# Kernel tuning notes

Hardware: AMD Instinct MI355X
Metric: run time of the kernel (lower is better)

The kernel has to match this reference:

```python
import jax, jax.numpy as jnp
import numpy as np

B, L, D, H = 1, 2048, 1024, 16
d = D // H  # head dim = 64


def setup_inputs() -> dict:
    key = jax.random.key(0)
    ks = jax.random.split(key, 8)
    s = 1.0 / np.sqrt(D)
    return {
        "x": jax.random.normal(ks[0], (B, L, D), jnp.float32),
        "Wqkv_w": (jax.random.normal(ks[1], (D, 3 * D), jnp.float32) * s),
        "Wqkv_b": jnp.zeros((3 * D,), jnp.float32),
        "out_w": (jax.random.normal(ks[2], (D, D), jnp.float32) * s),
        "out_b": jnp.zeros((D,), jnp.float32),
        "W_static": jnp.zeros((H, d, d), jnp.float32),
        "Lambda_raw": jax.random.uniform(ks[3], (H, d, d), jnp.float32, -3.0, 3.0),
        "Gamma": jax.random.uniform(ks[4], (H, d, d), jnp.float32, -0.5 / np.sqrt(d), 0.5 / np.sqrt(d)),
        "gate_w1": (jax.random.normal(ks[5], (D, D // 2), jnp.float32) * s),
        "gate_b1": jnp.zeros((D // 2,), jnp.float32),
        "gate_w2": (jax.random.normal(ks[6], (D // 2, H), jnp.float32) * (1.0 / np.sqrt(D // 2))),
        "gate_b2": jnp.zeros((H,), jnp.float32),
    }


def _forward(x, Wqkv_w, Wqkv_b, out_w, out_b, W_static, Lambda_raw, Gamma,
             gate_w1, gate_b1, gate_w2, gate_b2):
    Bb, Ll, Dm = x.shape
    Hh = Gamma.shape[0]
    dd = Dm // Hh
    scale = 1.0 / np.sqrt(dd)

    # qkv projection: (B,L,3D) -> (3, B, H, L, d) layout
    qkv = (x @ Wqkv_w + Wqkv_b).reshape(Bb, Ll, 3, Hh, dd)
    q = jnp.transpose(qkv[:, :, 0], (0, 2, 1, 3))  # (B,H,L,d)
    k = jnp.transpose(qkv[:, :, 1], (0, 2, 1, 3))
    v = jnp.transpose(qkv[:, :, 2], (0, 2, 1, 3))

    # --- softmax branch (causal, additive -10000 mask like the original) ---
    scores = jnp.einsum('bhid,bhjd->bhij', q, k) * scale
    causal_mask = jnp.triu(jnp.full((Ll, Ll), -10000.0, dtype=scores.dtype), 1)
    attn = jax.nn.softmax(scores + causal_mask, axis=-1)
    y_softmax = jnp.einsum('bhij,bhjd->bhid', attn, v)

    # --- STP branch: linear recurrence over time via lax.scan ---
    retention = 1.0 - jax.nn.sigmoid(Lambda_raw)  # (H,d,d)
    k_stp = k * scale

    def step(state, inp):
        q_t, k_t, v_t = inp  # each (B,H,d)
        hebbian = v_t[..., :, None] * k_t[..., None, :]          # (B,H,d,d)
        state = retention * state + Gamma * hebbian              # (B,H,d,d)
        y_t = jnp.einsum('bhij,bhj->bhi', W_static + state, q_t)  # (B,H,d)
        return state, y_t

    state0 = jnp.zeros((Bb, Hh, dd, dd), x.dtype)
    qT = jnp.moveaxis(q, 2, 0)      # (L,B,H,d)
    kT = jnp.moveaxis(k_stp, 2, 0)
    vT = jnp.moveaxis(v, 2, 0)
    _, ys = jax.lax.scan(step, state0, (qT, kT, vT))
    y_stp = jnp.moveaxis(ys, 0, 2)  # (B,H,L,d)

    # --- learned gate: Linear -> GELU(exact) -> Linear -> sigmoid ---
    g = jax.nn.gelu(x @ gate_w1 + gate_b1, approximate=False)
    alpha = jax.nn.sigmoid(g @ gate_w2 + gate_b2)        # (B,L,H)
    alpha = jnp.transpose(alpha, (0, 2, 1))[..., None]   # (B,H,L,1)

    y = alpha * y_softmax + (1.0 - alpha) * y_stp        # (B,H,L,d)
    y = jnp.transpose(y, (0, 2, 1, 3)).reshape(Bb, Ll, Dm)
    return y @ out_w + out_b


def reference(x, Wqkv_w, Wqkv_b, out_w, out_b, W_static, Lambda_raw, Gamma,
              gate_w1, gate_b1, gate_w2, gate_b2):
    return _forward(x, Wqkv_w, Wqkv_b, out_w, out_b, W_static, Lambda_raw,
                    Gamma, gate_w1, gate_b1, gate_w2, gate_b2)
```

## Files before the change

### kernel.cpp

```cpp
#include <hip/hip_runtime.h>
#include <hip/hip_bf16.h>

#define L_SEQ 2048
#define DMODEL 1024
#define NHEAD 16
#define DHEAD 64
#define D3 3072

typedef __attribute__((ext_vector_type(8))) short s8v;
typedef __attribute__((ext_vector_type(4))) float f4v;
typedef unsigned int u32;
#define AS1 __attribute__((address_space(1)))
#define AS3 __attribute__((address_space(3)))

__device__ __forceinline__ short f2bf(float f) {
  __hip_bfloat16 h = __float2bfloat16(f);
  return *reinterpret_cast<short*>(&h);
}
__device__ __forceinline__ float bf2f(short s) {
  return __uint_as_float(((u32)(unsigned short)s) << 16);
}
__device__ __forceinline__ int pack2bf(float lo, float hi) {
  return (int)(((unsigned)(unsigned short)f2bf(hi) << 16) |
               (unsigned)(unsigned short)f2bf(lo));
}

__global__ __launch_bounds__(256) void conv_x(const float* __restrict__ x,
                                              short* __restrict__ xb)
{
  int i = (blockIdx.x * 256 + threadIdx.x) * 4;
  float4 v = *(const float4*)(x + i);
  short4 o;
  o.x = f2bf(v.x); o.y = f2bf(v.y); o.z = f2bf(v.z); o.w = f2bf(v.w);
  *(short4*)(xb + i) = o;
}

__global__ __launch_bounds__(256) void transpose_conv(const float* __restrict__ W,
    short* __restrict__ Wt, int K, int N)
{
  __shared__ float T[32][33];
  int bx = blockIdx.x, by = blockIdx.y;
  int col = threadIdx.x & 31, rb = threadIdx.x >> 5;
  #pragma unroll
  for (int it = 0; it < 4; ++it) {
    int r = it * 8 + rb;
    T[r][col] = W[(size_t)(by * 32 + r) * N + bx * 32 + col];
  }
  __syncthreads();
  #pragma unroll
  for (int it = 0; it < 4; ++it) {
    int r = it * 8 + rb;
    Wt[(size_t)(bx * 32 + r) * K + by * 32 + col] = f2bf(T[col][r]);
  }
}

__global__ __launch_bounds__(256) void conv_vt(const float* __restrict__ Vf,
                                               short* __restrict__ Vtb)
{
  int kb = blockIdx.x, h = blockIdx.y;
  int tid = threadIdx.x;
  __shared__ float Vs[64][65];
  for (int idx = tid; idx < 2048; idx += 256) {
    int key = idx >> 5, e2 = idx & 31;
    float2 vv = *(const float2*)(Vf + (size_t)(kb * 64 + key) * 1024 + h * 64 + e2 * 2);
    Vs[key][e2 * 2] = vv.x; Vs[key][e2 * 2 + 1] = vv.y;
  }
  __syncthreads();
  for (int idx = tid; idx < 2048; idx += 256) {
    int dim = idx >> 5, k2 = idx & 31;
    *(int*)&Vtb[((size_t)h * 64 + dim) * 2048 + kb * 64 + k2 * 2] =
        pack2bf(Vs[k2 * 2][dim], Vs[k2 * 2 + 1][dim]);
  }
}

template<int BM, int BN, int MODE>
__global__ __launch_bounds__(256, 6) void gemm_mfma(
    const short* __restrict__ A, const short* __restrict__ Bt,
    const float* __restrict__ bias, const float* __restrict__ bias2,
    float* __restrict__ C, short* __restrict__ C2,
    short* __restrict__ QbP, short* __restrict__ KbP,
    int M, int N, int K)
{
  constexpr int LA = BM / 64, LB = BN / 64;
  constexpr int WM = BM / 2, WN = BN / 2;
  constexpr int MT = WM / 16, NT = WN / 16;
  __shared__ __align__(16) short As[2][BM * 32];
  __shared__ __align__(16) short Bs[2][BN * 32];
  const int tid = threadIdx.x;
  const int w = tid >> 6, lane = tid & 63;
  const int quad = lane >> 4, c = lane & 15;
  const int m0 = blockIdx.y * BM, n0 = blockIdx.x * BN;
  const int wm = (w & 1) * WM, wn = (w >> 1) * WN;
  f4v acc[MT][NT] = {};

  auto stage = [&](int buf, int k0) {
    #pragma unroll
    for (int it = 0; it < LA; ++it) {
      int off = (it * 256 + tid) * 16;
      int row = off >> 6, colh = (off & 63) >> 1;
      __builtin_amdgcn_global_load_lds(
          (const AS1 u32*)(A + (size_t)(m0 + row) * K + k0 + colh),
          (AS3 u32*)(&As[buf][0] + (off >> 1)), 16, 0, 0);
    }
    #pragma unroll
    for (int it = 0; it < LB; ++it) {
      int off = (it * 256 + tid) * 16;
      int row = off >> 6, colh = (off & 63) >> 1;
      __builtin_amdgcn_global_load_lds(
          (const AS1 u32*)(Bt + (size_t)(n0 + row) * K + k0 + colh),
          (AS3 u32*)(&Bs[buf][0] + (off >> 1)), 16, 0, 0);
    }
  };
  stage(0, 0);
  int cur = 0;
  for (int k0 = 0; k0 < K; k0 += 32) {
    __syncthreads();
    if (k0 + 32 < K) stage(cur ^ 1, k0 + 32);
    s8v af[MT], bf[NT];
    #pragma unroll
    for (int mt = 0; mt < MT; ++mt)
      af[mt] = *(s8v*)&As[cur][(wm + mt * 16 + c) * 32 + quad * 8];
    #pragma unroll
    for (int nt = 0; nt < NT; ++nt)
      bf[nt] = *(s8v*)&Bs[cur][(wn + nt * 16 + c) * 32 + quad * 8];
    #pragma unroll
    for (int mt = 0; mt < MT; ++mt)
      #pragma unroll
      for (int nt = 0; nt < NT; ++nt)
        acc[mt][nt] = __builtin_amdgcn_mfma_f32_16x16x32_bf16(
            af[mt], bf[nt], acc[mt][nt], 0, 0, 0);
    cur ^= 1;
  }
  #pragma unroll
  for (int mt = 0; mt < MT; ++mt)
    #pragma unroll
    for (int r = 0; r < 4; ++r) {
      int m = m0 + wm + mt * 16 + quad * 4 + r;
      #pragma unroll
      for (int nt = 0; nt < NT; ++nt) {
        int n = n0 + wn + nt * 16 + c;
        float v = acc[mt][nt][r];
        if (MODE == 0) {
          C[(size_t)m * N + n] = v + bias[n];
        } else {
          if (n < 2048) {
            float v2 = v + bias[n];
            int hh = (n >> 6) & 15, ee = n & 63;
            short* dst = (n < 1024) ? QbP : KbP;
            dst[((size_t)hh * 2048 + m) * 64 + ee] = f2bf(v2);
          } else if (n < 3072) {
            C[(size_t)m * 1024 + (n - 2048)] = v + bias[n];
          } else {
            float t = v + bias2[n - 3072];
            t = 0.5f * t * (1.0f + erff(t * 0.70710678118654752f));
            C2[(size_t)m * 512 + (n - 3072)] = f2bf(t);
          }
        }
      }
    }
}

__global__ __launch_bounds__(256) void attn_mfma(
    const short* __restrict__ Qb, const short* __restrict__ Kb,
    const short* __restrict__ Vtb, float* __restrict__ O0,
    float* __restrict__ O1, float* __restrict__ ml)
{
  const int bid = blockIdx.x;
  int h, qt, ts, te;
  float *Odst, *mdst, *ldst;
  if (bid < 512) {
    qt = 31 - (bid >> 5);
    int r = bid & 31; h = r >> 1;
    int n = qt + 1, n2 = (n + 1) >> 1;
    if ((r & 1) == 0) {
      ts = 0; te = n2;
      int s = h * 32 + qt;
      Odst = O0 + (size_t)s * 4096; mdst = ml + s * 64; ldst = ml + 32768 + s * 64;
    } else {
      ts = n2; te = n;
      int s = h * 16 + (qt - 16);
      Odst = O1 + (size_t)s * 4096; mdst = ml + 65536 + s * 64; ldst = ml + 81920 + s * 64;
    }
  } else {
    int r = bid - 512; qt = 15 - (r >> 4); h = r & 15; ts = 0; te = qt + 1;
    int s = h * 32 + qt;
    Odst = O0 + (size_t)s * 4096; mdst = ml + s * 64; ldst = ml + 32768 + s * 64;
  }
  const int q0 = qt * 64;
  const int tid = threadIdx.x;
  const int w = tid >> 6, lane = tid & 63;
  const int quad = lane >> 4, c = lane & 15;

  __shared__ __align__(16) char smem[27648];
  short* Ks = (short*)smem;
  short* Vt = Ks + 4608;
  short* Ps = Vt + 4608;
  float* Ob = (float*)smem;

  const int qrow = q0 + w * 16 + c;
  s8v qf[2];
  qf[0] = *(const s8v*)(Qb + ((size_t)h * 2048 + qrow) * 64 + quad * 8);
  qf[1] = *(const s8v*)(Qb + ((size_t)h * 2048 + qrow) * 64 + 32 + quad * 8);

  const int srow = tid >> 3, sc = (tid & 7) * 8;
  int4 pk0, pk1, pv0, pv1;
  auto load_tile = [&](int t0) {
    const short* kbase = Kb + ((size_t)h * 2048 + t0 * 64) * 64;
    const short* vbase = Vtb + (size_t)h * 64 * 2048 + t0 * 64;
    pk0 = *(const int4*)(kbase + (size_t)srow * 64 + sc);
    pk1 = *(const int4*)(kbase + (size_t)(srow + 32) * 64 + sc);
    pv0 = *(const int4*)(vbase + (size_t)srow * 2048 + sc);
    pv1 = *(const int4*)(vbase + (size_t)(srow + 32) * 2048 + sc);
  };
  load_tile(ts);

  f4v o_acc[4] = {};
  float m = -1e30f, l = 0.f;

  for (int t0 = ts; t0 < te; ++t0) {
    __syncthreads();
    *(int4*)&Ks[srow * 72 + sc] = pk0;
    *(int4*)&Ks[(srow + 32) * 72 + sc] = pk1;
    *(int4*)&Vt[srow * 72 + sc] = pv0;
    *(int4*)&Vt[(srow + 32) * 72 + sc] = pv1;
    __syncthreads();
    if (t0 + 1 < te) load_tile(t0 + 1);

    f4v s_acc[4] = {};
    #pragma unroll
    for (int kt = 0; kt < 4; ++kt) {
      #pragma unroll
      for (int kc = 0; kc < 2; ++kc) {
        s8v kf = *(s8v*)&Ks[(kt * 16 + c) * 72 + kc * 32 + quad * 8];
        s_acc[kt] = __builtin_amdgcn_mfma_f32_16x16x32_bf16(kf, qf[kc], s_acc[kt], 0, 0, 0);
      }
    }
    float sv[4][4];
    bool full = (t0 * 64 + 63) <= (q0 + w * 16);
    #pragma unroll
    for (int kt = 0; kt < 4; ++kt)
      #pragma unroll
      for (int r = 0; r < 4; ++r) {
        float s = s_acc[kt][r] * 0.125f;
        if (!full) {
          int key = t0 * 64 + kt * 16 + quad * 4 + r;
          s = (key <= qrow) ? s : -1e30f;
        }
        sv[kt][r] = s;
      }
    float mloc = -1e30f;
    #pragma unroll
    for (int kt = 0; kt < 4; ++kt)
      #pragma unroll
      for (int r = 0; r < 4; ++r) mloc = fmaxf(mloc, sv[kt][r]);
    mloc = fmaxf(mloc, __shfl_xor(mloc, 16));
    mloc = fmaxf(mloc, __shfl_xor(mloc, 32));
    float mnew = fmaxf(fmaxf(m, mloc), -1e20f);
    float alpha = __expf(m - mnew);
    m = mnew;
    float p[4][4], ls = 0.f;
    #pragma unroll
    for (int kt = 0; kt < 4; ++kt)
      #pragma unroll
      for (int r = 0; r < 4; ++r) { p[kt][r] = __expf(sv[kt][r] - mnew); ls += p[kt][r]; }
    ls += __shfl_xor(ls, 16);
    ls += __shfl_xor(ls, 32);
    l = l * alpha + ls;
    #pragma unroll
    for (int mt = 0; mt < 4; ++mt)
      #pragma unroll
      for (int r = 0; r < 4; ++r) o_acc[mt][r] *= alpha;
    short* Pw = Ps + w * 1152;
    #pragma unroll
    for (int kt = 0; kt < 4; ++kt) {
      *(int*)&Pw[c * 72 + kt * 16 + quad * 4]     = pack2bf(p[kt][0], p[kt][1]);
      *(int*)&Pw[c * 72 + kt * 16 + quad * 4 + 2] = pack2bf(p[kt][2], p[kt][3]);
    }
    #pragma unroll
    for (int kc2 = 0; kc2 < 2; ++kc2) {
      s8v pf = *(s8v*)&Pw[c * 72 + kc2 * 32 + quad * 8];
      #pragma unroll
      for (int mt = 0; mt < 4; ++mt) {
        s8v vf = *(s8v*)&Vt[(mt * 16 + c) * 72 + kc2 * 32 + quad * 8];
        o_acc[mt] = __builtin_amdgcn_mfma_f32_16x16x32_bf16(vf, pf, o_acc[mt], 0, 0, 0);
      }
    }
  }

  __syncthreads();
  #pragma unroll
  for (int mt = 0; mt < 4; ++mt)
    #pragma unroll
    for (int r = 0; r < 4; ++r)
      Ob[(w * 16 + c) * 66 + mt * 16 + quad * 4 + r] = o_acc[mt][r];
  if (quad == 0) { mdst[w * 16 + c] = m; ldst[w * 16 + c] = l; }
  __syncthreads();
  for (int i = tid; i < 4096; i += 256)
    Odst[i] = Ob[(i >> 6) * 66 + (i & 63)];
}

__global__ __launch_bounds__(256) void attn_merge(
    const float* __restrict__ O0, const float* __restrict__ O1,
    const float* __restrict__ ml, const float* __restrict__ ystp,
    const float* __restrict__ alpha, short* __restrict__ ycb)
{
  int bid = blockIdx.x;
  int h = bid >> 5, qt = bid & 31;
  int slot0 = h * 32 + qt;
  int tid = threadIdx.x;
  for (int it = 0; it < 16; ++it) {
    int idx = it * 256 + tid;
    int q = idx >> 6, e = idx & 63;
    int gq = qt * 64 + q;
    float oo = O0[(size_t)slot0 * 4096 + idx];
    float m0v = ml[slot0 * 64 + q], l0v = ml[32768 + slot0 * 64 + q];
    float ll;
    if (qt >= 16) {
      int slot1 = h * 16 + (qt - 16);
      float o1 = O1[(size_t)slot1 * 4096 + idx];
      float m1v = ml[65536 + slot1 * 64 + q], l1v = ml[81920 + slot1 * 64 + q];
      float ms = fmaxf(m0v, m1v);
      float w0 = __expf(m0v - ms), w1 = __expf(m1v - ms);
      oo = oo * w0 + o1 * w1;
      ll = l0v * w0 + l1v * w1;
    } else {
      ll = l0v;
    }
    float ys = oo / ll;
    float a = alpha[gq * 16 + h];
    float yst = ystp[((size_t)h * 2048 + gq) * 64 + e];
    ycb[(size_t)gq * 1024 + h * 64 + e] = f2bf(a * ys + (1.f - a) * yst);
  }
}

__global__ __launch_bounds__(256) void stp_local(const float* __restrict__ Vf,
    const short* __restrict__ Kb, const float* __restrict__ Lam,
    const float* __restrict__ Gam, float* __restrict__ states)
{
  int c = blockIdx.x, h = blockIdx.y;
  int tid = threadIdx.x;
  int i = tid >> 2, j0 = (tid & 3) * 16;
  __shared__ float Kc[64][64];
  __shared__ float Vc[64][64];
  for (int idx = tid; idx < 1024; idx += 256) {
    int t = idx >> 4, e4 = (idx & 15) * 4;
    short4 ks = *(const short4*)(Kb + ((size_t)h * 2048 + c * 64 + t) * 64 + e4);
    Kc[t][e4]     = bf2f(ks.x) * 0.125f;
    Kc[t][e4 + 1] = bf2f(ks.y) * 0.125f;
    Kc[t][e4 + 2] = bf2f(ks.z) * 0.125f;
    Kc[t][e4 + 3] = bf2f(ks.w) * 0.125f;
    float4 vv = *(const float4*)(Vf + (size_t)(c * 64 + t) * 1024 + h * 64 + e4);
    Vc[t][e4] = vv.x; Vc[t][e4 + 1] = vv.y; Vc[t][e4 + 2] = vv.z; Vc[t][e4 + 3] = vv.w;
  }
  float r[16], g[16], s[16];
  #pragma unroll
  for (int e = 0; e < 16; ++e) {
    int idx = h * 4096 + i * 64 + j0 + e;
    r[e] = 1.f / (1.f + expf(Lam[idx]));
    g[e] = Gam[idx];
    s[e] = 0.f;
  }
  __syncthreads();
  for (int t = 0; t < 64; ++t) {
    float v = Vc[t][i];
    #pragma unroll
    for (int e = 0; e < 16; ++e)
      s[e] = r[e] * s[e] + g[e] * (v * Kc[t][j0 + e]);
  }
  #pragma unroll
  for (int e = 0; e < 16; ++e)
    states[((size_t)h * 32 + c) * 4096 + i * 64 + j0 + e] = s[e];
}

__global__ __launch_bounds__(256) void stp_scan(const float* __restrict__ Lam,
                                                float* __restrict__ states)
{
  int gid = blockIdx.x * 256 + threadIdx.x;
  float r = 1.f / (1.f + expf(Lam[gid]));
  float r64 = r;
  #pragma unroll
  for (int q = 0; q < 6; ++q) r64 *= r64;
  int h = gid >> 12, low = gid & 4095;
  float acc = 0.f;
  for (int c = 0; c < 32; ++c) {
    size_t idx = ((size_t)h * 32 + c) * 4096 + low;
    float dloc = states[idx];
    states[idx] = acc;
    acc = r64 * acc + dloc;
  }
}

__global__ __launch_bounds__(256) void stp_out(const float* __restrict__ Vf,
    const short* __restrict__ Kb, const short* __restrict__ Qb,
    const float* __restrict__ Lam, const float* __restrict__ Gam,
    const float* __restrict__ Wst, const float* __restrict__ states,
    float* __restrict__ ystp)
{
  int c = blockIdx.x, h = blockIdx.y;
  int tid = threadIdx.x;
  int i = tid >> 2, j0 = (tid & 3) * 16;
  __shared__ float Kc[64][64];
  __shared__ float Vc[64][64];
  __shared__ float Qc[64][64];
  for (int idx = tid; idx < 1024; idx += 256) {
    int t = idx >> 4, e4 = (idx & 15) * 4;
    size_t bo = ((size_t)h * 2048 + c * 64 + t) * 64 + e4;
    short4 ks = *(const short4*)(Kb + bo);
    short4 qs = *(const short4*)(Qb + bo);
    Kc[t][e4]     = bf2f(ks.x) * 0.125f;
    Kc[t][e4 + 1] = bf2f(ks.y) * 0.125f;
    Kc[t][e4 + 2] = bf2f(ks.z) * 0.125f;
    Kc[t][e4 + 3] = bf2f(ks.w) * 0.125f;
    Qc[t][e4]     = bf2f(qs.x);
    Qc[t][e4 + 1] = bf2f(qs.y);
    Qc[t][e4 + 2] = bf2f(qs.z);
    Qc[t][e4 + 3] = bf2f(qs.w);
    float4 vv = *(const float4*)(Vf + (size_t)(c * 64 + t) * 1024 + h * 64 + e4);
    Vc[t][e4] = vv.x; Vc[t][e4 + 1] = vv.y; Vc[t][e4 + 2] = vv.z; Vc[t][e4 + 3] = vv.w;
  }
  float r[16], g[16], s[16], w[16];
  #pragma unroll
  for (int e = 0; e < 16; ++e) {
    int idx = h * 4096 + i * 64 + j0 + e;
    r[e] = 1.f / (1.f + expf(Lam[idx]));
    g[e] = Gam[idx];
    w[e] = Wst[idx];
    s[e] = states[((size_t)h * 32 + c) * 4096 + i * 64 + j0 + e];
  }
  __syncthreads();
  for (int t = 0; t < 64; ++t) {
    float v = Vc[t][i];
    float y = 0.f;
    #pragma unroll
    for (int e = 0; e < 16; ++e) {
      s[e] = r[e] * s[e] + g[e] * (v * Kc[t][j0 + e]);
      y += (w[e] + s[e]) * Qc[t][j0 + e];
    }
    y += __shfl_xor(y, 1);
    y += __shfl_xor(y, 2);
    if ((tid & 3) == 0)
      ystp[((size_t)h * L_SEQ + c * 64 + t) * 64 + i] = y;
  }
}

__global__ __launch_bounds__(256) void gate2_kernel(const short* __restrict__ g_bf,
    const float* __restrict__ w2, const float* __restrict__ b2,
    float* __restrict__ alpha)
{
  int gid = blockIdx.x * 256 + threadIdx.x;
  int l = gid >> 4, h = gid & 15;
  float acc = b2[h];
  const short* grow = g_bf + (size_t)l * 512;
  for (int c2 = 0; c2 < 512; c2 += 2) {
    u32 pk = *(const u32*)(grow + c2);
    float g0 = __uint_as_float(pk << 16);
    float g1 = __uint_as_float(pk & 0xffff0000u);
    acc += g0 * w2[c2 * 16 + h] + g1 * w2[(c2 + 1) * 16 + h];
  }
  alpha[gid] = 1.f / (1.f + expf(-acc));
}

extern "C" void kernel_launch(void* const* d_in, const int* in_sizes, int n_in,
                              void* d_out, int out_size, void* d_ws, size_t ws_size,
                              hipStream_t stream) {
  (void)in_sizes; (void)n_in; (void)out_size; (void)ws_size;
  const float* x      = (const float*)d_in[0];
  const float* Wqkv_w = (const float*)d_in[1];
  const float* Wqkv_b = (const float*)d_in[2];
  const float* out_w  = (const float*)d_in[3];
  const float* out_b  = (const float*)d_in[4];
  const float* W_st   = (const float*)d_in[5];
  const float* Lam    = (const float*)d_in[6];
  const float* Gam    = (const float*)d_in[7];
  const float* gw1    = (const float*)d_in[8];
  const float* gb1    = (const float*)d_in[9];
  const float* gw2    = (const float*)d_in[10];
  const float* gb2    = (const float*)d_in[11];

  float* ws     = (float*)d_ws;
  float* Vf     = ws;
  float* O0buf  = ws + 2097152;
  float* ystp   = ws + 4194304;
  float* states = ws + 6291456;
  float* ovl    = ws + 8388608;
  float* alpha  = ws + 12058624;
  float* ml     = ws + 12091392;
  short* Qb     = (short*)(ws + 12189696);
  short* Kb     = Qb + 2097152;
  short* xb     = (short*)ovl;
  short* wt_buf = (short*)(ovl + 1048576);
  short* g_bf   = (short*)(ovl + 2883584);
  short* Vtb    = (short*)ovl;
  short* wtO    = (short*)ovl;
  float* O1buf  = states;
  short* ycb    = (short*)(states + 1048576);

  conv_x<<<dim3(2048), 256, 0, stream>>>(x, xb);
  transpose_conv<<<dim3(96, 32), 256, 0, stream>>>(Wqkv_w, wt_buf, 1024, 3072);
  transpose_conv<<<dim3(16, 32), 256, 0, stream>>>(gw1, wt_buf + 3072 * 1024, 1024, 512);
  gemm_mfma<64, 64, 2><<<dim3(56, 32), 256, 0, stream>>>(
      xb, wt_buf, Wqkv_b, gb1, Vf, g_bf, Qb, Kb, 2048, 3584, 1024);
  gate2_kernel<<<dim3(128), 256, 0, stream>>>(g_bf, gw2, gb2, alpha);
  stp_local<<<dim3(32, 16), 256, 0, stream>>>(Vf, Kb, Lam, Gam, states);
  stp_scan<<<dim3(256), 256, 0, stream>>>(Lam, states);
  stp_out<<<dim3(32, 16), 256, 0, stream>>>(Vf, Kb, Qb, Lam, Gam, W_st, states, ystp);
  conv_vt<<<dim3(32, 16), 256, 0, stream>>>(Vf, Vtb);
  attn_mfma<<<dim3(768), 256, 0, stream>>>(Qb, Kb, Vtb, O0buf, O1buf, ml);
  attn_merge<<<dim3(512), 256, 0, stream>>>(O0buf, O1buf, ml, ystp, alpha, ycb);
  transpose_conv<<<dim3(32, 32), 256, 0, stream>>>(out_w, wtO, 1024, 1024);
  gemm_mfma<64, 64, 0><<<dim3(16, 32), 256, 0, stream>>>(
      ycb, wtO, out_b, nullptr, (float*)d_out, nullptr, nullptr, nullptr, 2048, 1024, 1024);
}
```

Before: 264.1 us.

## Fuse input and weight conversion kernels into one prep launch, enlarge QKV GEMM tile

Merges the x bf16 conversion and the three weight transpose-convert kernels into a single launch, with block ranges dispatching to each job. The out_w transpose now runs up front, so its result gets its own workspace region instead of reusing the overlap buffer. The QKV+gate GEMM switches to a 128-row tile with half the grid in M. This cuts launch count and gaps between launches, and the larger tile improves reuse, but the GEMM now runs fewer blocks (896 vs 1792), which may hurt occupancy. It also needs a larger workspace.

```diff
diff --git a/kernel.cpp b/kernel.cpp
--- a/kernel.cpp
+++ b/kernel.cpp
@@ -25,22 +25,11 @@
                (unsigned)(unsigned short)f2bf(lo));
 }
 
-__global__ __launch_bounds__(256) void conv_x(const float* __restrict__ x,
-                                              short* __restrict__ xb)
-{
-  int i = (blockIdx.x * 256 + threadIdx.x) * 4;
-  float4 v = *(const float4*)(x + i);
-  short4 o;
-  o.x = f2bf(v.x); o.y = f2bf(v.y); o.z = f2bf(v.z); o.w = f2bf(v.w);
-  *(short4*)(xb + i) = o;
-}
-
-__global__ __launch_bounds__(256) void transpose_conv(const float* __restrict__ W,
-    short* __restrict__ Wt, int K, int N)
+__device__ __forceinline__ void transpose32(const float* __restrict__ W,
+    short* __restrict__ Wt, int K, int N, int bx, int by, int tid)
 {
   __shared__ float T[32][33];
-  int bx = blockIdx.x, by = blockIdx.y;
-  int col = threadIdx.x & 31, rb = threadIdx.x >> 5;
+  int col = tid & 31, rb = tid >> 5;
   #pragma unroll
   for (int it = 0; it < 4; ++it) {
     int r = it * 8 + rb;
@@ -51,6 +40,31 @@
   for (int it = 0; it < 4; ++it) {
     int r = it * 8 + rb;
     Wt[(size_t)(bx * 32 + r) * K + by * 32 + col] = f2bf(T[col][r]);
+  }
+}
+
+__global__ __launch_bounds__(256) void prep_kernel(
+    const float* __restrict__ x, short* __restrict__ xb,
+    const float* __restrict__ Wqkv_w, const float* __restrict__ gw1,
+    const float* __restrict__ out_w, short* __restrict__ wt_buf,
+    short* __restrict__ wtO)
+{
+  int b = blockIdx.x, tid = threadIdx.x;
+  if (b < 2048) {
+    int i = (b * 256 + tid) * 4;
+    float4 v = *(const float4*)(x + i);
+    short4 o;
+    o.x = f2bf(v.x); o.y = f2bf(v.y); o.z = f2bf(v.z); o.w = f2bf(v.w);
+    *(short4*)(xb + i) = o;
+  } else if (b < 5120) {
+    int r = b - 2048;
+    transpose32(Wqkv_w, wt_buf, 1024, 3072, r % 96, r / 96, tid);
+  } else if (b < 5632) {
+    int r = b - 5120;
+    transpose32(gw1, wt_buf + 3072 * 1024, 1024, 512, r % 16, r / 16, tid);
+  } else {
+    int r = b - 5632;
+    transpose32(out_w, wtO, 1024, 1024, r % 32, r / 32, tid);
   }
 }
 
@@ -487,18 +501,16 @@
   float* ml     = ws + 12091392;
   short* Qb     = (short*)(ws + 12189696);
   short* Kb     = Qb + 2097152;
+  short* wtO    = (short*)(ws + 14286848);
   short* xb     = (short*)ovl;
   short* wt_buf = (short*)(ovl + 1048576);
   short* g_bf   = (short*)(ovl + 2883584);
   short* Vtb    = (short*)ovl;
-  short* wtO    = (short*)ovl;
   float* O1buf  = states;
   short* ycb    = (short*)(states + 1048576);
 
-  conv_x<<<dim3(2048), 256, 0, stream>>>(x, xb);
-  transpose_conv<<<dim3(96, 32), 256, 0, stream>>>(Wqkv_w, wt_buf, 1024, 3072);
-  transpose_conv<<<dim3(16, 32), 256, 0, stream>>>(gw1, wt_buf + 3072 * 1024, 1024, 512);
-  gemm_mfma<64, 64, 2><<<dim3(56, 32), 256, 0, stream>>>(
+  prep_kernel<<<dim3(6656), 256, 0, stream>>>(x, xb, Wqkv_w, gw1, out_w, wt_buf, wtO);
+  gemm_mfma<128, 64, 2><<<dim3(56, 16), 256, 0, stream>>>(
       xb, wt_buf, Wqkv_b, gb1, Vf, g_bf, Qb, Kb, 2048, 3584, 1024);
   gate2_kernel<<<dim3(128), 256, 0, stream>>>(g_bf, gw2, gb2, alpha);
   stp_local<<<dim3(32, 16), 256, 0, stream>>>(Vf, Kb, Lam, Gam, states);
@@ -507,7 +519,6 @@
   conv_vt<<<dim3(32, 16), 256, 0, stream>>>(Vf, Vtb);
   attn_mfma<<<dim3(768), 256, 0, stream>>>(Qb, Kb, Vtb, O0buf, O1buf, ml);
   attn_merge<<<dim3(512), 256, 0, stream>>>(O0buf, O1buf, ml, ystp, alpha, ycb);
-  transpose_conv<<<dim3(32, 32), 256, 0, stream>>>(out_w, wtO, 1024, 1024);
   gemm_mfma<64, 64, 0><<<dim3(16, 32), 256, 0, stream>>>(
       ycb, wtO, out_b, nullptr, (float*)d_out, nullptr, nullptr, nullptr, 2048, 1024, 1024);
 }
```

Result: faster. 257.5 us (-2.5%).
